# Optimization experiments

Measured on AMD Instinct MI355X. Metric: run time of the kernel, lower is better.

The kernel has to match this reference:

```python
import jax, jax.numpy as jnp
import numpy as np

LAMBDA = 0.5
WINDOW = 2
NUM_SCALES = 2
EPS = 1e-5


def setup_inputs() -> dict:
    key = jax.random.key(0)
    ks = jax.random.split(key, 9)
    N, C, T, Vw = 32, 96, 300, 50
    V = 25
    out_c = 192
    return {
        "x": jax.random.normal(ks[0], (N, C, T, Vw), jnp.float32),
        "xx": jax.random.normal(ks[1], (N, 3, 300, V), jnp.float32),
        "A_res": jax.random.normal(ks[2], (Vw, Vw), jnp.float32) * 1e-6,
        "W": jax.random.normal(ks[3], (out_c, NUM_SCALES * C), jnp.float32) * 0.05,
        "b": jax.random.normal(ks[4], (out_c,), jnp.float32) * 0.01,
        "gamma": jnp.ones((out_c,), jnp.float32),
        "beta": jnp.zeros((out_c,), jnp.float32),
        "running_mean": jax.random.normal(ks[5], (out_c,), jnp.float32) * 0.01,
        "running_var": jax.random.uniform(ks[6], (out_c,), jnp.float32, 0.5, 1.5),
    }


def reference(x, xx, A_res, W, b, gamma, beta, running_mean, running_var):
    # xx: (N, 3, 300, V) -> (N, T=300, V, C=3)
    xxp = jnp.transpose(xx, (0, 2, 3, 1))
    # pairwise squared L2 distances (norm then squared in exp == sum of squares)
    diff = xxp[:, :, :, None, :] - xxp[:, :, None, :, :]      # (N,T,V,V,3)
    dists2 = jnp.sum(diff * diff, axis=-1)                     # (N,T,V,V)
    A_dsg = jnp.exp(-dists2 / LAMBDA)
    # conv3d with (1,1,300,1,1) kernel of 1/300 == mean over the 300 frames
    A_t = jnp.mean(A_dsg, axis=1)                              # (N,V,V)
    # per-sample symmetric normalization D^-1/2 A D^-1/2
    deg = jnp.sum(A_t, axis=-1)                                # (N,V)
    dinv = deg ** -0.5
    A_norm = A_t * dinv[:, :, None] * dinv[:, None, :]
    # kron-style repeat to spatial-temporal graph (N, V*window, V*window)
    A_large = jnp.tile(A_norm, (1, WINDOW, WINDOW))
    A = A_large + A_res                                        # (N,Vw,Vw)
    # conv2d with (1,N,1,1) kernel of 1/N == mean over the batch
    A_scale = jnp.mean(A, axis=0)                              # (Vw,Vw)
    # graph conv
    agg = jnp.einsum('vu,nctu->nctv', A_scale, x)              # (N,C,T,Vw)
    N, C, T, Vw = x.shape
    Vs = Vw // NUM_SCALES
    agg = agg.reshape(N, C, T, NUM_SCALES, Vs)
    agg = jnp.transpose(agg, (0, 3, 1, 2, 4)).reshape(N, NUM_SCALES * C, T, Vs)
    # MLP: 1x1 conv + BN (activation='linear')
    out = jnp.einsum('oc,nctv->notv', W, agg) + b[None, :, None, None]
    scale = gamma * jax.lax.rsqrt(running_var + EPS)
    out = out * scale[None, :, None, None] + (beta - running_mean * scale)[None, :, None, None]
    return jax.nn.relu(out)
```

## Files before the change

### kernel.cpp

```cpp
#include <hip/hip_runtime.h>
#include <hip/hip_bf16.h>

typedef __attribute__((ext_vector_type(8))) short short8;
typedef __attribute__((ext_vector_type(4))) short short4v;
typedef __attribute__((ext_vector_type(4))) float f32x4;
typedef __attribute__((ext_vector_type(2))) float f32x2;

__device__ __forceinline__ unsigned short f2bf(float f) {
    unsigned int u = __builtin_bit_cast(unsigned int, f);
    u += 0x7fffu + ((u >> 16) & 1u);
    return (unsigned short)(u >> 16);
}
__device__ __forceinline__ unsigned int pack2(float a, float b) {
    union { __hip_bfloat162 h; unsigned int u; } r;
    r.h = __float22bfloat162_rn(make_float2(a, b));
    return r.u;
}
__device__ __forceinline__ short4v cvt4(float a, float b, float c, float d) {
    union { __hip_bfloat162 h[2]; short4v s; } u;
    u.h[0] = __float22bfloat162_rn(make_float2(a, b));
    u.h[1] = __float22bfloat162_rn(make_float2(c, d));
    return u.s;
}

__global__ void kA(const float* __restrict__ xx, float* __restrict__ At_part) {
    __shared__ float xs3[3][60][25];
    const int tc = blockIdx.x, n = blockIdx.y;
    const int tid = threadIdx.x;
    const float* base = xx + (size_t)n * 22500 + tc * 1500;
    for (int idx = tid; idx < 4500; idx += 256) {
        int ch = idx / 1500, rt = idx % 1500;
        xs3[ch][rt / 25][rt % 25] = base[ch * 7500 + rt];
    }
    __syncthreads();
    for (int p = tid; p < 625; p += 256) {
        int v = p / 25, u = p % 25;
        float s = 0.f;
        for (int t = 0; t < 60; ++t) {
            float dx = xs3[0][t][v] - xs3[0][t][u];
            float dy = xs3[1][t][v] - xs3[1][t][u];
            float dz = xs3[2][t][v] - xs3[2][t][u];
            s += __expf(-2.f * (dx * dx + dy * dy + dz * dz));
        }
        At_part[(size_t)(n * 5 + tc) * 625 + p] = s;
    }
}

__global__ void kB1(const float* __restrict__ At_part, float* __restrict__ Acontrib) {
    __shared__ float At[625];
    __shared__ float dinv[25];
    const int n = blockIdx.x, tid = threadIdx.x;
    for (int p = tid; p < 625; p += 256) {
        float s = 0.f;
        for (int tc = 0; tc < 5; ++tc) s += At_part[(size_t)(n * 5 + tc) * 625 + p];
        At[p] = s;
    }
    __syncthreads();
    if (tid < 25) {
        float d = 0.f;
        for (int u = 0; u < 25; ++u) d += At[tid * 25 + u];
        dinv[tid] = rsqrtf(d * (1.f / 300.f));
    }
    __syncthreads();
    for (int p = tid; p < 625; p += 256)
        Acontrib[n * 625 + p] = At[p] * (1.f / 300.f) * dinv[p / 25] * dinv[p % 25] * (1.f / 32.f);
}

__global__ void kB2(const float* __restrict__ Acontrib, const float* __restrict__ A_res,
                    const float* __restrict__ W, const float* __restrict__ b,
                    const float* __restrict__ gamma, const float* __restrict__ beta,
                    const float* __restrict__ rm, const float* __restrict__ rv,
                    short* __restrict__ bsTg, short* __restrict__ Wpg,
                    float* __restrict__ bbg) {
    const int tid = threadIdx.x;
    if (blockIdx.x == 0) {
        __shared__ float macc[625];
        for (int p = tid; p < 625; p += 256) {
            float s = 0.f;
            for (int n = 0; n < 32; ++n) s += Acontrib[n * 625 + p];
            macc[p] = s;
        }
        __syncthreads();
        for (int idx = tid; idx < 64 * 72; idx += 256) {
            int col = idx / 72, u = idx % 72;
            float v = 0.f;
            if (col < 50 && u < 50) v = macc[(col % 25) * 25 + (u % 25)] + A_res[col * 50 + u];
            bsTg[idx] = (short)f2bf(v);
        }
        if (tid < 192) {
            float sc = gamma[tid] * rsqrtf(rv[tid] + 1e-5f);
            bbg[tid] = b[tid] * sc + beta[tid] - rm[tid] * sc;
        }
    } else {
        const int e = (blockIdx.x - 1) * 1024 + tid * 4;
        const int o = e / 192;
        const float sc = gamma[o] * rsqrtf(rv[o] + 1e-5f);
        float4 w = *(const float4*)(W + e);
        short4v s4 = { (short)f2bf(w.x * sc), (short)f2bf(w.y * sc),
                       (short)f2bf(w.z * sc), (short)f2bf(w.w * sc) };
        *(short4v*)(Wpg + e) = s4;
    }
}

__device__ __forceinline__ void ldx(const float* __restrict__ x, int gbase,
                                    f32x2 (&pf)[7], int tid) {
#pragma unroll
    for (int i = 0; i < 7; ++i) {
        int idx = i * 384 + tid;
        idx = idx < 2400 ? idx : 2399;
        int c = idx / 25, q = idx - c * 25;
        pf[i] = *(const f32x2*)(x + gbase + c * 15000 + 2 * q);
    }
}
__device__ __forceinline__ void stx(char* xsb, int slot, const f32x2 (&pf)[7], int tid) {
#pragma unroll
    for (int i = 0; i < 7; ++i) {
        int idx = i * 384 + tid;
        if (idx < 2400) {
            int c = idx / 25, q = idx - c * 25;
            *(unsigned int*)(xsb + ((slot * 12288 + c * 128 + q * 4) ^ ((c & 7) << 4)))
                = pack2(pf[i].x, pf[i].y);
        }
    }
}

__global__ __launch_bounds__(384, 3)
void kC(const float* __restrict__ x, const short* __restrict__ Wpg,
        const short* __restrict__ bsTg, const float* __restrict__ bbg,
        float* __restrict__ out) {
    __shared__ __align__(16) char xsb[2 * 12288];
    __shared__ __align__(16) short bsT[64 * 72];
    __shared__ __align__(16) short a2T[2][32][208];

    const int tid = threadIdx.x;
    const int lane = tid & 63;
    const int wid = tid >> 6;
    const int lam = lane & 15;
    const int kc = (lane >> 4) * 8;
    const int cb = (lane >> 4) * 4;
    const int n = blockIdx.y;
    const int t0 = blockIdx.x * 4;
    const int gb0 = n * 1440000 + t0 * 50;
    const int cgl = wid * 16 + lam;

    f32x2 pf2[13];
#pragma unroll
    for (int i = 0; i < 13; ++i) {
        int idx = i * 384 + tid;
        idx = idx < 4800 ? idx : 4799;
        int c = idx / 50, q2 = idx - c * 50;
        int tl = q2 >= 25, q = q2 - 25 * tl;
        pf2[i] = *(const f32x2*)(x + gb0 + c * 15000 + tl * 50 + 2 * q);
    }

    short8 wf[2][6];
#pragma unroll
    for (int ot = 0; ot < 2; ++ot)
#pragma unroll
        for (int ks = 0; ks < 6; ++ks)
            wf[ot][ks] = *(const short8*)(Wpg + ((2 * wid + ot) * 16 + lam) * 192 + ks * 32 + kc);

    float bb[2];
#pragma unroll
    for (int ot = 0; ot < 2; ++ot) bb[ot] = bbg[(2 * wid + ot) * 16 + lam];

    {
        const int4* src = (const int4*)bsTg;
        int4* dst = (int4*)bsT;
        for (int i = tid; i < 576; i += 384) dst[i] = src[i];
    }
    for (int idx = tid; idx < 1344; idx += 384) {
        int r = idx / 7, k = idx - r * 7;
        int slot = r / 96, c = r - 96 * slot;
        *(unsigned int*)(xsb + ((slot * 12288 + c * 128 + (50 + 2 * k) * 2) ^ ((c & 7) << 4))) = 0;
    }
    for (int idx = tid; idx < 1456; idx += 384) {
        int buf = idx / 728, rem = idx - buf * 728;
        int row = 25 + rem / 104, col2 = rem - (rem / 104) * 104;
        *((unsigned int*)&a2T[buf][row][0] + col2) = 0;
    }
#pragma unroll
    for (int i = 0; i < 13; ++i) {
        int idx = i * 384 + tid;
        if (idx < 4800) {
            int c = idx / 50, q2 = idx - c * 50;
            int tl = q2 >= 25, q = q2 - 25 * tl;
            *(unsigned int*)(xsb + ((tl * 12288 + c * 128 + q * 4) ^ ((c & 7) << 4)))
                = pack2(pf2[i].x, pf2[i].y);
        }
    }
    asm volatile("s_waitcnt lgkmcnt(0)" ::: "memory");
    __builtin_amdgcn_s_barrier();

    const f32x4 z = {0.f, 0.f, 0.f, 0.f};
    f32x2 pf[7];

#pragma unroll 1
    for (int tl = 0; tl < 4; ++tl) {
        const int slot = tl & 1;
        short* a2w = &a2T[slot][0][0];

        if (tl < 2) ldx(x, gb0 + (tl + 2) * 50, pf, tid);

        short8 xb[2];
#pragma unroll
        for (int ks = 0; ks < 2; ++ks)
            xb[ks] = *(const short8*)(xsb +
                ((slot * 12288 + cgl * 128 + (ks * 32 + kc) * 2) ^ ((cgl & 7) << 4)));
        f32x4 acc1[4];
#pragma unroll
        for (int m = 0; m < 4; ++m) acc1[m] = z;
#pragma unroll
        for (int ks = 0; ks < 2; ++ks)
#pragma unroll
            for (int m = 0; m < 4; ++m) {
                const short8 af = *(const short8*)(bsT + (m * 16 + lam) * 72 + ks * 32 + kc);
                acc1[m] = __builtin_amdgcn_mfma_f32_16x16x32_bf16(af, xb[ks], acc1[m], 0, 0, 0);
            }

#pragma unroll
        for (int m = 0; m < 3; ++m) {
            short4v sv = cvt4(acc1[m][0], acc1[m][1], acc1[m][2], acc1[m][3]);
#pragma unroll
            for (int r = 0; r < 4; ++r) {
                const int v = m * 16 + cb + r;
                const int s = v >= 25;
                a2w[(v - 25 * s) * 208 + s * 96 + cgl] = sv[r];
            }
        }
        if (cb == 0) {
            a2w[23 * 208 + 96 + cgl] = (short)f2bf(acc1[3][0]);
            a2w[24 * 208 + 96 + cgl] = (short)f2bf(acc1[3][1]);
        }

        asm volatile("s_waitcnt lgkmcnt(0)" ::: "memory");
        __builtin_amdgcn_s_barrier();

        f32x4 acc2[2][2];
#pragma unroll
        for (int g = 0; g < 2; ++g) { acc2[g][0] = z; acc2[g][1] = z; }
#pragma unroll
        for (int ks = 0; ks < 6; ++ks) {
            const short8 A0 = *(const short8*)(a2w + lam * 208 + ks * 32 + kc);
            const short8 A1 = *(const short8*)(a2w + (16 + lam) * 208 + ks * 32 + kc);
#pragma unroll
            for (int ot = 0; ot < 2; ++ot) {
                acc2[0][ot] = __builtin_amdgcn_mfma_f32_16x16x32_bf16(A0, wf[ot][ks], acc2[0][ot], 0, 0, 0);
                acc2[1][ot] = __builtin_amdgcn_mfma_f32_16x16x32_bf16(A1, wf[ot][ks], acc2[1][ot], 0, 0, 0);
            }
        }

        if (tl < 2) stx(xsb, slot, pf, tid);

        const int t = t0 + tl;
#pragma unroll
        for (int ot = 0; ot < 2; ++ot) {
            const int o = (2 * wid + ot) * 16 + lam;
            float* op = out + ((size_t)(n * 192 + o) * 300 + t) * 25;
#pragma unroll
            for (int r = 0; r < 4; ++r) {
                float vv = acc2[0][ot][r] + bb[ot];
                op[cb + r] = vv > 0.f ? vv : 0.f;
            }
#pragma unroll
            for (int r = 0; r < 4; ++r) {
                const int tv = 16 + cb + r;
                if (tv < 25) {
                    float vv = acc2[1][ot][r] + bb[ot];
                    op[tv] = vv > 0.f ? vv : 0.f;
                }
            }
        }
    }
}

extern "C" void kernel_launch(void* const* d_in, const int* in_sizes, int n_in,
                              void* d_out, int out_size, void* d_ws, size_t ws_size,
                              hipStream_t stream) {
    const float* x     = (const float*)d_in[0];
    const float* xx    = (const float*)d_in[1];
    const float* A_res = (const float*)d_in[2];
    const float* W     = (const float*)d_in[3];
    const float* b     = (const float*)d_in[4];
    const float* gamma = (const float*)d_in[5];
    const float* beta  = (const float*)d_in[6];
    const float* rm    = (const float*)d_in[7];
    const float* rv    = (const float*)d_in[8];
    float* out = (float*)d_out;

    char* ws = (char*)d_ws;
    float* At_part  = (float*)ws;
    float* Acontrib = (float*)(ws + 400000);
    short* bsTg     = (short*)(ws + 480000);
    short* Wpg      = (short*)(ws + 489216);
    float* bbg      = (float*)(ws + 562944);

    kA<<<dim3(5, 32), 256, 0, stream>>>(xx, At_part);
    kB1<<<32, 256, 0, stream>>>(At_part, Acontrib);
    kB2<<<37, 256, 0, stream>>>(Acontrib, A_res, W, b, gamma, beta, rm, rv, bsTg, Wpg, bbg);
    kC<<<dim3(75, 32), 384, 0, stream>>>(x, Wpg, bsTg, bbg, out);
}
```

Measured before the change: 181.5 us.

## Split fused graph-conv/MLP kernel into two kernels via bf16 intermediate buffer

```diff
diff --git a/kernel.cpp b/kernel.cpp
--- a/kernel.cpp
+++ b/kernel.cpp
@@ -102,6 +102,22 @@
     }
 }
 
+__global__ void kB2b(const float* __restrict__ W, const float* __restrict__ gamma,
+                     const float* __restrict__ rv, short* __restrict__ Wfrag) {
+    const int idx = blockIdx.x * 256 + threadIdx.x;
+    const int ot = idx / 384, r = idx - ot * 384;
+    const int ks = r / 64, lane = r - ks * 64;
+    const int o = ot * 16 + (lane & 15);
+    const int k0 = ks * 32 + (lane >> 4) * 8;
+    const float sc = gamma[o] * rsqrtf(rv[o] + 1e-5f);
+    float4 w0 = *(const float4*)(W + o * 192 + k0);
+    float4 w1 = *(const float4*)(W + o * 192 + k0 + 4);
+    union { short4v h[2]; short8 v; } u;
+    u.h[0] = cvt4(w0.x * sc, w0.y * sc, w0.z * sc, w0.w * sc);
+    u.h[1] = cvt4(w1.x * sc, w1.y * sc, w1.z * sc, w1.w * sc);
+    *(short8*)(Wfrag + (size_t)idx * 8) = u.v;
+}
+
 __device__ __forceinline__ void ldx(const float* __restrict__ x, int gbase,
                                     f32x2 (&pf)[7], int tid) {
 #pragma unroll
@@ -152,18 +168,15 @@
         int tl = q2 >= 25, q = q2 - 25 * tl;
         pf2[i] = *(const f32x2*)(x + gb0 + c * 15000 + tl * 50 + 2 * q);
     }
-
     short8 wf[2][6];
 #pragma unroll
     for (int ot = 0; ot < 2; ++ot)
 #pragma unroll
         for (int ks = 0; ks < 6; ++ks)
             wf[ot][ks] = *(const short8*)(Wpg + ((2 * wid + ot) * 16 + lam) * 192 + ks * 32 + kc);
-
     float bb[2];
 #pragma unroll
     for (int ot = 0; ot < 2; ++ot) bb[ot] = bbg[(2 * wid + ot) * 16 + lam];
-
     {
         const int4* src = (const int4*)bsTg;
         int4* dst = (int4*)bsT;
@@ -199,7 +212,6 @@
     for (int tl = 0; tl < 4; ++tl) {
         const int slot = tl & 1;
         short* a2w = &a2T[slot][0][0];
-
         if (tl < 2) ldx(x, gb0 + (tl + 2) * 50, pf, tid);
 
         short8 xb[2];
@@ -217,7 +229,6 @@
                 const short8 af = *(const short8*)(bsT + (m * 16 + lam) * 72 + ks * 32 + kc);
                 acc1[m] = __builtin_amdgcn_mfma_f32_16x16x32_bf16(af, xb[ks], acc1[m], 0, 0, 0);
             }
-
 #pragma unroll
         for (int m = 0; m < 3; ++m) {
             short4v sv = cvt4(acc1[m][0], acc1[m][1], acc1[m][2], acc1[m][3]);
@@ -232,7 +243,6 @@
             a2w[23 * 208 + 96 + cgl] = (short)f2bf(acc1[3][0]);
             a2w[24 * 208 + 96 + cgl] = (short)f2bf(acc1[3][1]);
         }
-
         asm volatile("s_waitcnt lgkmcnt(0)" ::: "memory");
         __builtin_amdgcn_s_barrier();
 
@@ -249,7 +259,6 @@
                 acc2[1][ot] = __builtin_amdgcn_mfma_f32_16x16x32_bf16(A1, wf[ot][ks], acc2[1][ot], 0, 0, 0);
             }
         }
-
         if (tl < 2) stx(xsb, slot, pf, tid);
 
         const int t = t0 + tl;
@@ -269,6 +278,190 @@
                     float vv = acc2[1][ot][r] + bb[ot];
                     op[tv] = vv > 0.f ? vv : 0.f;
                 }
+            }
+        }
+    }
+}
+
+__global__ __launch_bounds__(384, 3)
+void kC1(const float* __restrict__ x, const short* __restrict__ bsTg,
+         short* __restrict__ agg2) {
+    __shared__ __align__(16) char xsb[2 * 12288];
+    __shared__ __align__(16) short bsT[64 * 72];
+    __shared__ __align__(16) short a2T[2][32][208];
+
+    const int tid = threadIdx.x;
+    const int lane = tid & 63;
+    const int wid = tid >> 6;
+    const int lam = lane & 15;
+    const int kc = (lane >> 4) * 8;
+    const int cb = (lane >> 4) * 4;
+    const int n = blockIdx.y;
+    const int t0 = blockIdx.x * 4;
+    const int gb0 = n * 1440000 + t0 * 50;
+    const int cgl = wid * 16 + lam;
+
+    f32x2 pf2[13];
+#pragma unroll
+    for (int i = 0; i < 13; ++i) {
+        int idx = i * 384 + tid;
+        idx = idx < 4800 ? idx : 4799;
+        int c = idx / 50, q2 = idx - c * 50;
+        int tl = q2 >= 25, q = q2 - 25 * tl;
+        pf2[i] = *(const f32x2*)(x + gb0 + c * 15000 + tl * 50 + 2 * q);
+    }
+    {
+        const int4* src = (const int4*)bsTg;
+        int4* dst = (int4*)bsT;
+        for (int i = tid; i < 576; i += 384) dst[i] = src[i];
+    }
+    for (int idx = tid; idx < 1344; idx += 384) {
+        int r = idx / 7, k = idx - r * 7;
+        int slot = r / 96, c = r - 96 * slot;
+        *(unsigned int*)(xsb + ((slot * 12288 + c * 128 + (50 + 2 * k) * 2) ^ ((c & 7) << 4))) = 0;
+    }
+#pragma unroll
+    for (int i = 0; i < 13; ++i) {
+        int idx = i * 384 + tid;
+        if (idx < 4800) {
+            int c = idx / 50, q2 = idx - c * 50;
+            int tl = q2 >= 25, q = q2 - 25 * tl;
+            *(unsigned int*)(xsb + ((tl * 12288 + c * 128 + q * 4) ^ ((c & 7) << 4)))
+                = pack2(pf2[i].x, pf2[i].y);
+        }
+    }
+    asm volatile("s_waitcnt lgkmcnt(0)" ::: "memory");
+    __builtin_amdgcn_s_barrier();
+
+    const f32x4 z = {0.f, 0.f, 0.f, 0.f};
+    f32x2 pf[7];
+
+#pragma unroll 1
+    for (int tl = 0; tl < 4; ++tl) {
+        const int slot = tl & 1;
+        short* a2w = &a2T[slot][0][0];
+        if (tl < 2) ldx(x, gb0 + (tl + 2) * 50, pf, tid);
+
+        short8 xb[2];
+#pragma unroll
+        for (int ks = 0; ks < 2; ++ks)
+            xb[ks] = *(const short8*)(xsb +
+                ((slot * 12288 + cgl * 128 + (ks * 32 + kc) * 2) ^ ((cgl & 7) << 4)));
+        f32x4 acc1[4];
+#pragma unroll
+        for (int m = 0; m < 4; ++m) acc1[m] = z;
+#pragma unroll
+        for (int ks = 0; ks < 2; ++ks)
+#pragma unroll
+            for (int m = 0; m < 4; ++m) {
+                const short8 af = *(const short8*)(bsT + (m * 16 + lam) * 72 + ks * 32 + kc);
+                acc1[m] = __builtin_amdgcn_mfma_f32_16x16x32_bf16(af, xb[ks], acc1[m], 0, 0, 0);
+            }
+#pragma unroll
+        for (int m = 0; m < 3; ++m) {
+            short4v sv = cvt4(acc1[m][0], acc1[m][1], acc1[m][2], acc1[m][3]);
+#pragma unroll
+            for (int r = 0; r < 4; ++r) {
+                const int v = m * 16 + cb + r;
+                const int s = v >= 25;
+                a2w[(v - 25 * s) * 208 + s * 96 + cgl] = sv[r];
+            }
+        }
+        if (cb == 0) {
+            a2w[23 * 208 + 96 + cgl] = (short)f2bf(acc1[3][0]);
+            a2w[24 * 208 + 96 + cgl] = (short)f2bf(acc1[3][1]);
+        }
+        asm volatile("s_waitcnt lgkmcnt(0)" ::: "memory");
+        __builtin_amdgcn_s_barrier();
+
+        {
+            const unsigned int* a2d = (const unsigned int*)a2w;
+            unsigned int* dst = (unsigned int*)agg2
+                + (size_t)n * 720000 + (size_t)(t0 + tl) * 2400;
+#pragma unroll
+            for (int i = 0; i < 7; ++i) {
+                int idx = i * 384 + tid;
+                if (idx < 2400) {
+                    int v = idx / 96, c2 = idx - v * 96;
+                    dst[v * 96 + c2] = a2d[v * 104 + c2];
+                }
+            }
+        }
+        if (tl < 2) stx(xsb, slot, pf, tid);
+    }
+}
+
+__global__ __launch_bounds__(256, 3)
+void kC2(const short* __restrict__ agg2, const short* __restrict__ Wfrag,
+         const float* __restrict__ bbg, float* __restrict__ out) {
+    __shared__ __align__(16) unsigned int asb[64 * 100];
+
+    const int tid = threadIdx.x;
+    const int lane = tid & 63;
+    const int wid = tid >> 6;
+    const int lam = lane & 15;
+    const int kc = (lane >> 4) * 8;
+    const int cb = (lane >> 4) * 4;
+    const int n = blockIdx.y;
+    const int tv0 = blockIdx.x * 64;
+
+    short8 wf[3][6];
+    float bb[3];
+#pragma unroll
+    for (int j = 0; j < 3; ++j) {
+        const int ot = wid * 3 + j;
+#pragma unroll
+        for (int ks = 0; ks < 6; ++ks)
+            wf[j][ks] = *(const short8*)(Wfrag + ((size_t)(ot * 6 + ks) * 64 + lane) * 8);
+        bb[j] = bbg[ot * 16 + lam];
+    }
+
+    {
+        const unsigned int* src = (const unsigned int*)agg2 + (size_t)n * 720000;
+#pragma unroll
+        for (int k = 0; k < 24; ++k) {
+            int d = k * 256 + tid;
+            int row = d / 96, c2 = d - row * 96;
+            int tvg = tv0 + row;
+            tvg = tvg < 7500 ? tvg : 7499;
+            asb[row * 100 + c2] = src[(size_t)tvg * 96 + c2];
+        }
+    }
+    __syncthreads();
+
+    const f32x4 z = {0.f, 0.f, 0.f, 0.f};
+    f32x4 acc[4][3];
+#pragma unroll
+    for (int m = 0; m < 4; ++m)
+#pragma unroll
+        for (int j = 0; j < 3; ++j) acc[m][j] = z;
+
+#pragma unroll
+    for (int ks = 0; ks < 6; ++ks) {
+        short8 a[4];
+#pragma unroll
+        for (int m = 0; m < 4; ++m)
+            a[m] = *(const short8*)((const short*)asb + (m * 16 + lam) * 200 + ks * 32 + kc);
+#pragma unroll
+        for (int m = 0; m < 4; ++m)
+#pragma unroll
+            for (int j = 0; j < 3; ++j)
+                acc[m][j] = __builtin_amdgcn_mfma_f32_16x16x32_bf16(a[m], wf[j][ks], acc[m][j], 0, 0, 0);
+    }
+
+#pragma unroll
+    for (int m = 0; m < 4; ++m) {
+        const int tvg = tv0 + m * 16 + cb;
+        if (tvg < 7500) {
+#pragma unroll
+            for (int j = 0; j < 3; ++j) {
+                const int o = (wid * 3 + j) * 16 + lam;
+                float4 v;
+                v.x = acc[m][j][0] + bb[j]; v.x = v.x > 0.f ? v.x : 0.f;
+                v.y = acc[m][j][1] + bb[j]; v.y = v.y > 0.f ? v.y : 0.f;
+                v.z = acc[m][j][2] + bb[j]; v.z = v.z > 0.f ? v.z : 0.f;
+                v.w = acc[m][j][3] + bb[j]; v.w = v.w > 0.f ? v.w : 0.f;
+                *(float4*)(out + (size_t)(n * 192 + o) * 7500 + tvg) = v;
             }
         }
     }
@@ -294,9 +487,19 @@
     short* bsTg     = (short*)(ws + 480000);
     short* Wpg      = (short*)(ws + 489216);
     float* bbg      = (float*)(ws + 562944);
+    short* Wfrag    = (short*)(ws + 563712);
+    short* agg2     = (short*)(ws + 637440);
+    const bool bigws = ws_size >= (size_t)637440 + 92160000u;
 
     kA<<<dim3(5, 32), 256, 0, stream>>>(xx, At_part);
     kB1<<<32, 256, 0, stream>>>(At_part, Acontrib);
     kB2<<<37, 256, 0, stream>>>(Acontrib, A_res, W, b, gamma, beta, rm, rv, bsTg, Wpg, bbg);
-    kC<<<dim3(75, 32), 384, 0, stream>>>(x, Wpg, bsTg, bbg, out);
-}
+    kB2b<<<18, 256, 0, stream>>>(W, gamma, rv, Wfrag);
+
+    if (bigws) {
+        kC1<<<dim3(75, 32), 384, 0, stream>>>(x, bsTg, agg2);
+        kC2<<<dim3(118, 32), 256, 0, stream>>>(agg2, Wfrag, bbg, out);
+    } else {
+        kC<<<dim3(75, 32), 384, 0, stream>>>(x, Wpg, bsTg, bbg, out);
+    }
+}
```

Result: no change. 182.7 us (+0.7%).
